# Performance work log

Measured on AMD Instinct MI355X. Metric: run time of the kernel, lower is better.

## Reference

```python
import jax, jax.numpy as jnp
import numpy as np
import math

D_MODEL, D_K, D_V, H = 512, 64, 64, 8

def setup_inputs() -> dict:
    key = jax.random.key(0)
    ks = jax.random.split(key, 8)
    B, L = 2, 4096
    q = jax.random.normal(ks[0], (B, L, D_MODEL), dtype=jnp.float32)
    k = jax.random.normal(ks[1], (B, L, D_MODEL), dtype=jnp.float32)
    v = jax.random.normal(ks[2], (B, L, D_MODEL), dtype=jnp.float32)
    attention_mask = jnp.ones((B, L), dtype=jnp.int32)
    s = 1.0 / math.sqrt(D_MODEL)
    Wq = jax.random.uniform(ks[3], (D_MODEL, H * D_K), dtype=jnp.float32, minval=-s, maxval=s)
    Wk = jax.random.uniform(ks[4], (D_MODEL, H * D_K), dtype=jnp.float32, minval=-s, maxval=s)
    Wv = jax.random.uniform(ks[5], (D_MODEL, H * D_V), dtype=jnp.float32, minval=-s, maxval=s)
    so = 1.0 / math.sqrt(H * D_V)
    Wo = jax.random.uniform(ks[6], (H * D_V, D_MODEL), dtype=jnp.float32, minval=-so, maxval=so)
    return {"q": q, "k": k, "v": v, "attention_mask": attention_mask,
            "Wq": Wq, "Wk": Wk, "Wv": Wv, "Wo": Wo}

def reference(q, k, v, attention_mask, Wq, Wk, Wv, Wo):
    B, L, _ = q.shape
    scale = 1.0 / math.sqrt(D_K)
    # project and split heads: [B, H, L, d]
    qh = (q @ Wq).reshape(B, L, H, D_K).transpose(0, 2, 1, 3)
    kh = (k @ Wk).reshape(B, L, H, D_K).transpose(0, 2, 1, 3)
    vh = (v @ Wv).reshape(B, L, H, D_V).transpose(0, 2, 1, 3)
    score = jnp.einsum('bhqd,bhkd->bhqk', qh, kh) * scale  # [B,H,L,L]
    mask = attention_mask[:, None, None, :]  # [B,1,1,L]
    score = jnp.where(mask == 0, -jnp.inf, score)
    attn = jax.nn.softmax(score, axis=-1)
    out = jnp.einsum('bhqk,bhkd->bhqd', attn, vh)
    out = out.transpose(0, 2, 1, 3).reshape(B, L, H * D_V)
    return out @ Wo
```

## Files before the change

kernel.cpp:

```cpp
#include <hip/hip_runtime.h>

typedef short bf16x8 __attribute__((ext_vector_type(8)));
typedef float f32x4 __attribute__((ext_vector_type(4)));
typedef unsigned short u16x8 __attribute__((ext_vector_type(8)));

static __device__ __forceinline__ unsigned short f2bf(float f) {
  unsigned int x = __builtin_bit_cast(unsigned int, f);
  x += 0x7FFFu + ((x >> 16) & 1u);
  return (unsigned short)(x >> 16);
}
static __device__ __forceinline__ unsigned int pk2bf(float a, float b) {
  unsigned int ia = __builtin_bit_cast(unsigned int, a) + 0x8000u;
  unsigned int ib = __builtin_bit_cast(unsigned int, b) + 0x8000u;
  return __builtin_amdgcn_perm(ib, ia, 0x07060302u);
}
static __device__ __forceinline__ void gl2lds16(const unsigned short* g, unsigned short* l) {
  __builtin_amdgcn_global_load_lds(
      (const __attribute__((address_space(1))) unsigned int*)g,
      (__attribute__((address_space(3))) unsigned int*)l, 16, 0, 0);
}

__global__ __launch_bounds__(256) void cvt3(const float* __restrict__ q, const float* __restrict__ k,
                                            const float* __restrict__ v,
                                            unsigned short* __restrict__ qo, unsigned short* __restrict__ ko,
                                            unsigned short* __restrict__ vo) {
  const float* src = (blockIdx.y == 0) ? q : (blockIdx.y == 1) ? k : v;
  unsigned short* dst = (blockIdx.y == 0) ? qo : (blockIdx.y == 1) ? ko : vo;
  int i = (blockIdx.x * 256 + threadIdx.x) * 8;
  float4 a = *(const float4*)(src + i);
  float4 b = *(const float4*)(src + i + 4);
  uint4 pk;
  pk.x = pk2bf(a.x, a.y); pk.y = pk2bf(a.z, a.w);
  pk.z = pk2bf(b.x, b.y); pk.w = pk2bf(b.z, b.w);
  *(uint4*)(dst + i) = pk;
}

__global__ __launch_bounds__(256) void wtrans4(const float* __restrict__ Wq, const float* __restrict__ Wk,
                                               const float* __restrict__ Wv, const float* __restrict__ Wo,
                                               unsigned short* __restrict__ WT) {
  __shared__ __align__(16) float T[64 * 68];
  const int z = blockIdx.z;
  const float* W = (z == 0) ? Wq : (z == 1) ? Wk : (z == 2) ? Wv : Wo;
  unsigned short* out = WT + (size_t)z * 512 * 512;
  const int k0 = blockIdx.x * 64, n0 = blockIdx.y * 64;
  const int tid = threadIdx.x;
#pragma unroll
  for (int i = 0; i < 4; ++i) {
    int chunk = i * 256 + tid;
    int row = chunk >> 4, fc = chunk & 15;
    *(float4*)(T + row * 68 + fc * 4) =
        *(const float4*)(W + (size_t)(k0 + row) * 512 + n0 + fc * 4);
  }
  __syncthreads();
#pragma unroll
  for (int i = 0; i < 2; ++i) {
    int chunk = i * 256 + tid;
    int nr = chunk >> 3, kc = chunk & 7;
    u16x8 v;
#pragma unroll
    for (int j = 0; j < 8; ++j) v[j] = f2bf(T[(kc * 8 + j) * 68 + nr]);
    *(u16x8*)(out + (size_t)(n0 + nr) * 512 + k0 + kc * 8) = v;
  }
}

__global__ __launch_bounds__(256) void gemm_qkv(const unsigned short* __restrict__ Aq,
                                                const unsigned short* __restrict__ Ak,
                                                const unsigned short* __restrict__ Av,
                                                const unsigned short* __restrict__ Bt,
                                                unsigned short* __restrict__ C,
                                                float qscale) {
  __shared__ __align__(16) unsigned short Abuf[2][128 * 64];
  __shared__ __align__(16) unsigned short Bbuf[2][64 * 64];
  const int K = 512, LDC = 1536;
  const unsigned short* A = (blockIdx.y < 8) ? Aq : (blockIdx.y < 16) ? Ak : Av;
  const float scale = (blockIdx.y < 8) ? qscale : 1.0f;
  const int tid = threadIdx.x;
  const int wid = tid >> 6, lane = tid & 63, quad = lane >> 4, li = lane & 15;
  const int bm = blockIdx.x * 128, bn = blockIdx.y * 64;
  const int wm = wid * 32;
  const unsigned short* ga[4]; int oa[4];
  const unsigned short* gb[2]; int ob[2];
#pragma unroll
  for (int i = 0; i < 4; ++i) {
    int lam = i * 256 + wid * 64 + lane;
    int r = lam >> 3, c = (lam & 7) ^ (r & 7);
    ga[i] = A + (size_t)(bm + r) * K + c * 8;
    oa[i] = lam * 8;
  }
#pragma unroll
  for (int i = 0; i < 2; ++i) {
    int lam = i * 256 + wid * 64 + lane;
    int r = lam >> 3, c = (lam & 7) ^ (r & 7);
    gb[i] = Bt + (size_t)(bn + r) * K + c * 8;
    ob[i] = lam * 8;
  }
#pragma unroll
  for (int i = 0; i < 4; ++i) { gl2lds16(ga[i], &Abuf[0][oa[i]]); ga[i] += 64; }
#pragma unroll
  for (int i = 0; i < 2; ++i) { gl2lds16(gb[i], &Bbuf[0][ob[i]]); gb[i] += 64; }

  f32x4 acc[2][4] = {};
  const int sw = li & 7;
  for (int s = 0; s < 8; ++s) {
    __builtin_amdgcn_s_barrier();
    if (s + 1 < 8) {
      int p = (s + 1) & 1;
#pragma unroll
      for (int i = 0; i < 4; ++i) { gl2lds16(ga[i], &Abuf[p][oa[i]]); ga[i] += 64; }
#pragma unroll
      for (int i = 0; i < 2; ++i) { gl2lds16(gb[i], &Bbuf[p][ob[i]]); gb[i] += 64; }
      asm volatile("s_waitcnt vmcnt(6)" ::: "memory");
    } else {
      asm volatile("s_waitcnt vmcnt(0)" ::: "memory");
    }
    __builtin_amdgcn_s_barrier();
    __builtin_amdgcn_sched_barrier(0);
    const unsigned short* As = &Abuf[s & 1][0];
    const unsigned short* Bs = &Bbuf[s & 1][0];
#pragma unroll
    for (int kk = 0; kk < 2; ++kk) {
      bf16x8 af[2], bfr[4];
#pragma unroll
      for (int t = 0; t < 2; ++t)
        af[t] = *(const bf16x8*)(As + (wm + t * 16 + li) * 64 + (((kk * 4 + quad) ^ sw) * 8));
#pragma unroll
      for (int t = 0; t < 4; ++t)
        bfr[t] = *(const bf16x8*)(Bs + (t * 16 + li) * 64 + (((kk * 4 + quad) ^ sw) * 8));
#pragma unroll
      for (int mt = 0; mt < 2; ++mt)
#pragma unroll
        for (int nt = 0; nt < 4; ++nt)
          acc[mt][nt] = __builtin_amdgcn_mfma_f32_16x16x32_bf16(af[mt], bfr[nt], acc[mt][nt], 0, 0, 0);
    }
  }
#pragma unroll
  for (int mt = 0; mt < 2; ++mt)
#pragma unroll
    for (int nt = 0; nt < 4; ++nt) {
      int r0 = bm + wm + mt * 16 + quad * 4;
      int c  = bn + nt * 16 + li;
#pragma unroll
      for (int r = 0; r < 4; ++r)
        C[(size_t)(r0 + r) * LDC + c] = f2bf(acc[mt][nt][r] * scale);
    }
}

__global__ __launch_bounds__(256) void gemm_o(const unsigned short* __restrict__ A,
                                              const unsigned short* __restrict__ Bt,
                                              float* __restrict__ Cf) {
  __shared__ __align__(16) unsigned short Abuf[2][128 * 64];
  __shared__ __align__(16) unsigned short Bbuf[2][64 * 64];
  const int K = 512, LDC = 512;
  const int tid = threadIdx.x;
  const int wid = tid >> 6, lane = tid & 63, quad = lane >> 4, li = lane & 15;
  const int bm = blockIdx.x * 128, bn = blockIdx.y * 64;
  const int wm = wid * 32;
  const unsigned short* ga[4]; int oa[4];
  const unsigned short* gb[2]; int ob[2];
#pragma unroll
  for (int i = 0; i < 4; ++i) {
    int lam = i * 256 + wid * 64 + lane;
    int r = lam >> 3, c = (lam & 7) ^ (r & 7);
    ga[i] = A + (size_t)(bm + r) * K + c * 8;
    oa[i] = lam * 8;
  }
#pragma unroll
  for (int i = 0; i < 2; ++i) {
    int lam = i * 256 + wid * 64 + lane;
    int r = lam >> 3, c = (lam & 7) ^ (r & 7);
    gb[i] = Bt + (size_t)(bn + r) * K + c * 8;
    ob[i] = lam * 8;
  }
#pragma unroll
  for (int i = 0; i < 4; ++i) { gl2lds16(ga[i], &Abuf[0][oa[i]]); ga[i] += 64; }
#pragma unroll
  for (int i = 0; i < 2; ++i) { gl2lds16(gb[i], &Bbuf[0][ob[i]]); gb[i] += 64; }

  f32x4 acc[2][4] = {};
  const int sw = li & 7;
  for (int s = 0; s < 8; ++s) {
    __builtin_amdgcn_s_barrier();
    if (s + 1 < 8) {
      int p = (s + 1) & 1;
#pragma unroll
      for (int i = 0; i < 4; ++i) { gl2lds16(ga[i], &Abuf[p][oa[i]]); ga[i] += 64; }
#pragma unroll
      for (int i = 0; i < 2; ++i) { gl2lds16(gb[i], &Bbuf[p][ob[i]]); gb[i] += 64; }
      asm volatile("s_waitcnt vmcnt(6)" ::: "memory");
    } else {
      asm volatile("s_waitcnt vmcnt(0)" ::: "memory");
    }
    __builtin_amdgcn_s_barrier();
    __builtin_amdgcn_sched_barrier(0);
    const unsigned short* As = &Abuf[s & 1][0];
    const unsigned short* Bs = &Bbuf[s & 1][0];
#pragma unroll
    for (int kk = 0; kk < 2; ++kk) {
      bf16x8 af[2], bfr[4];
#pragma unroll
      for (int t = 0; t < 2; ++t)
        af[t] = *(const bf16x8*)(As + (wm + t * 16 + li) * 64 + (((kk * 4 + quad) ^ sw) * 8));
#pragma unroll
      for (int t = 0; t < 4; ++t)
        bfr[t] = *(const bf16x8*)(Bs + (t * 16 + li) * 64 + (((kk * 4 + quad) ^ sw) * 8));
#pragma unroll
      for (int mt = 0; mt < 2; ++mt)
#pragma unroll
        for (int nt = 0; nt < 4; ++nt)
          acc[mt][nt] = __builtin_amdgcn_mfma_f32_16x16x32_bf16(af[mt], bfr[nt], acc[mt][nt], 0, 0, 0);
    }
  }
#pragma unroll
  for (int mt = 0; mt < 2; ++mt)
#pragma unroll
    for (int nt = 0; nt < 4; ++nt) {
      int r0 = bm + wm + mt * 16 + quad * 4;
      int c  = bn + nt * 16 + li;
#pragma unroll
      for (int r = 0; r < 4; ++r)
        Cf[(size_t)(r0 + r) * LDC + c] = acc[mt][nt][r];
    }
}

__global__ __launch_bounds__(256) void vtrans(const unsigned short* __restrict__ qkv,
                                              unsigned short* __restrict__ vt) {
  __shared__ __align__(16) unsigned short T[64 * 72];
  const int kt = blockIdx.x;
  const int bh = blockIdx.y;
  const int b = bh >> 3, h = bh & 7;
  const int tid = threadIdx.x;
#pragma unroll
  for (int i = 0; i < 2; ++i) {
    int chunk = i * 256 + tid;
    int row = chunk >> 3, c8 = chunk & 7;
    *(uint4*)(T + row * 72 + c8 * 8) =
        *(const uint4*)(qkv + (size_t)(b * 4096 + kt * 64 + row) * 1536 + 1024 + h * 64 + c8 * 8);
  }
  __syncthreads();
#pragma unroll
  for (int i = 0; i < 2; ++i) {
    int chunk = i * 256 + tid;
    int dr = chunk >> 3, c8 = chunk & 7;
    u16x8 v;
#pragma unroll
    for (int j = 0; j < 8; ++j) {
      int p = c8 * 8 + j;
      int ph = p & 31;
      int lk = (p & 32) | (((ph >> 2) & 1) << 4) | (((ph >> 3) & 3) << 2) | (ph & 3);
      v[j] = T[lk * 72 + dr];
    }
    *(u16x8*)(vt + (size_t)(bh * 64 + dr) * 4096 + kt * 64 + c8 * 8) = v;
  }
}

__global__ __launch_bounds__(256) void attn(const unsigned short* __restrict__ qkv,
                                            const unsigned short* __restrict__ vt,
                                            const int* __restrict__ mask,
                                            unsigned short* __restrict__ obuf) {
  __shared__ __align__(16) unsigned short Kbuf[2][64 * 64];
  __shared__ __align__(16) unsigned short Vbuf[2][64 * 64];
  __shared__ __align__(16) unsigned short MskBits[256];
  const int qt = blockIdx.x, h = blockIdx.y, b = blockIdx.z;
  const int tid = threadIdx.x;
  const int wid = tid >> 6, lane = tid & 63, quad = lane >> 4, li = lane & 15;
  const size_t tok0 = (size_t)b * 4096;

  {
    const int4* mp = (const int4*)(mask + b * 4096 + tid * 16);
    unsigned int bits = 0;
#pragma unroll
    for (int j = 0; j < 4; ++j) {
      int4 m4 = mp[j];
      bits |= (m4.x ? 1u : 0u) << (j * 4 + 0);
      bits |= (m4.y ? 1u : 0u) << (j * 4 + 1);
      bits |= (m4.z ? 1u : 0u) << (j * 4 + 2);
      bits |= (m4.w ? 1u : 0u) << (j * 4 + 3);
    }
    MskBits[tid] = (unsigned short)bits;
  }

  const unsigned short* qp0 = qkv + (tok0 + qt * 128 + wid * 32 + li) * 1536 + h * 64;
  const unsigned short* qp1 = qp0 + (size_t)16 * 1536;
  bf16x8 bq[2][2];
  bq[0][0] = *(const bf16x8*)(qp0 + quad * 8);
  bq[0][1] = *(const bf16x8*)(qp0 + 32 + quad * 8);
  bq[1][0] = *(const bf16x8*)(qp1 + quad * 8);
  bq[1][1] = *(const bf16x8*)(qp1 + 32 + quad * 8);

  const unsigned short* kbase = qkv + tok0 * 1536 + 512 + h * 64;
  const unsigned short* vbase = vt + (size_t)(b * 8 + h) * 64 * 4096;
  const int l0 = tid,       sr0 = l0 >> 3, sc0 = (l0 & 7) ^ (sr0 & 7);
  const int l1 = 256 + tid, sr1 = l1 >> 3, sc1 = (l1 & 7) ^ (sr1 & 7);
  const unsigned short* gk0 = kbase + (size_t)sr0 * 1536 + sc0 * 8;
  const unsigned short* gk1 = kbase + (size_t)sr1 * 1536 + sc1 * 8;
  const unsigned short* gv0 = vbase + (size_t)sr0 * 4096 + sc0 * 8;
  const unsigned short* gv1 = vbase + (size_t)sr1 * 4096 + sc1 * 8;
  const int ok0 = l0 * 8, ok1 = l1 * 8;

  gl2lds16(gk0, &Kbuf[0][ok0]); gl2lds16(gk1, &Kbuf[0][ok1]);
  gl2lds16(gv0, &Vbuf[0][ok0]); gl2lds16(gv1, &Vbuf[0][ok1]);
  gk0 += (size_t)64 * 1536; gk1 += (size_t)64 * 1536; gv0 += 64; gv1 += 64;

  f32x4 lacc[2] = {};
  f32x4 accO[2][4] = {};
  const int sw = li & 7;

  asm volatile("s_waitcnt lgkmcnt(0)" ::: "memory");

  for (int t = 0; t < 64; ++t) {
    __builtin_amdgcn_s_barrier();
    if (t < 63) {
      int p = (t + 1) & 1;
      gl2lds16(gk0, &Kbuf[p][ok0]); gl2lds16(gk1, &Kbuf[p][ok1]);
      gl2lds16(gv0, &Vbuf[p][ok0]); gl2lds16(gv1, &Vbuf[p][ok1]);
      gk0 += (size_t)64 * 1536; gk1 += (size_t)64 * 1536; gv0 += 64; gv1 += 64;
      asm volatile("s_waitcnt vmcnt(4)" ::: "memory");
    } else {
      asm volatile("s_waitcnt vmcnt(0)" ::: "memory");
    }
    __builtin_amdgcn_s_barrier();
    __builtin_amdgcn_sched_barrier(0);
    const unsigned short* Ks = &Kbuf[t & 1][0];
    const unsigned short* Vs = &Vbuf[t & 1][0];

    f32x4 s[2][4];
    __builtin_amdgcn_s_setprio(1);
#pragma unroll
    for (int kb = 0; kb < 4; ++kb) {
      const unsigned short* kr = Ks + (kb * 16 + li) * 64;
      bf16x8 ak0 = *(const bf16x8*)(kr + ((quad ^ sw) * 8));
      bf16x8 ak1 = *(const bf16x8*)(kr + (((4 + quad) ^ sw) * 8));
#pragma unroll
      for (int qg = 0; qg < 2; ++qg) {
        f32x4 z = {};
        z = __builtin_amdgcn_mfma_f32_16x16x32_bf16(ak0, bq[qg][0], z, 0, 0, 0);
        z = __builtin_amdgcn_mfma_f32_16x16x32_bf16(ak1, bq[qg][1], z, 0, 0, 0);
        s[qg][kb] = z;
      }
    }
    __builtin_amdgcn_s_setprio(0);
    unsigned long long mbits = *(const unsigned long long*)(MskBits + t * 4);
    if (mbits != ~0ull) {
#pragma unroll
      for (int kb = 0; kb < 4; ++kb)
#pragma unroll
        for (int r = 0; r < 4; ++r) {
          int key = kb * 16 + quad * 4 + r;
          if (!((mbits >> key) & 1ull)) { s[0][kb][r] = -1e30f; s[1][kb][r] = -1e30f; }
        }
    }
    bf16x8 pf[2][2];
#pragma unroll
    for (int qg = 0; qg < 2; ++qg) {
#pragma unroll
      for (int kb = 0; kb < 4; ++kb) {
#pragma unroll
        for (int r = 0; r < 4; ++r) s[qg][kb][r] = __builtin_amdgcn_exp2f(s[qg][kb][r]);
        lacc[qg] += s[qg][kb];
      }
      uint4 u0, u1;
      u0.x = pk2bf(s[qg][0][0], s[qg][0][1]); u0.y = pk2bf(s[qg][0][2], s[qg][0][3]);
      u0.z = pk2bf(s[qg][1][0], s[qg][1][1]); u0.w = pk2bf(s[qg][1][2], s[qg][1][3]);
      u1.x = pk2bf(s[qg][2][0], s[qg][2][1]); u1.y = pk2bf(s[qg][2][2], s[qg][2][3]);
      u1.z = pk2bf(s[qg][3][0], s[qg][3][1]); u1.w = pk2bf(s[qg][3][2], s[qg][3][3]);
      pf[qg][0] = __builtin_bit_cast(bf16x8, u0);
      pf[qg][1] = __builtin_bit_cast(bf16x8, u1);
    }
    __builtin_amdgcn_s_setprio(1);
#pragma unroll
    for (int dc = 0; dc < 4; ++dc) {
      const unsigned short* vr = Vs + (dc * 16 + li) * 64;
      bf16x8 bv0 = *(const bf16x8*)(vr + ((quad ^ sw) * 8));
      bf16x8 bv1 = *(const bf16x8*)(vr + (((4 + quad) ^ sw) * 8));
#pragma unroll
      for (int qg = 0; qg < 2; ++qg) {
        accO[qg][dc] = __builtin_amdgcn_mfma_f32_16x16x32_bf16(pf[qg][0], bv0, accO[qg][dc], 0, 0, 0);
        accO[qg][dc] = __builtin_amdgcn_mfma_f32_16x16x32_bf16(pf[qg][1], bv1, accO[qg][dc], 0, 0, 0);
      }
    }
    __builtin_amdgcn_s_setprio(0);
  }
#pragma unroll
  for (int qg = 0; qg < 2; ++qg) {
    float lt = lacc[qg][0] + lacc[qg][1] + lacc[qg][2] + lacc[qg][3];
    lt += __shfl_xor(lt, 16);
    lt += __shfl_xor(lt, 32);
    float lv0 = 1.f / __shfl(lt, quad * 4 + 0);
    float lv1 = 1.f / __shfl(lt, quad * 4 + 1);
    float lv2 = 1.f / __shfl(lt, quad * 4 + 2);
    float lv3 = 1.f / __shfl(lt, quad * 4 + 3);
    size_t r0q = tok0 + qt * 128 + wid * 32 + qg * 16 + quad * 4;
#pragma unroll
    for (int dc = 0; dc < 4; ++dc) {
      size_t col = h * 64 + dc * 16 + li;
      obuf[(r0q + 0) * 512 + col] = f2bf(accO[qg][dc][0] * lv0);
      obuf[(r0q + 1) * 512 + col] = f2bf(accO[qg][dc][1] * lv1);
      obuf[(r0q + 2) * 512 + col] = f2bf(accO[qg][dc][2] * lv2);
      obuf[(r0q + 3) * 512 + col] = f2bf(accO[qg][dc][3] * lv3);
    }
  }
}

extern "C" void kernel_launch(void* const* d_in, const int* in_sizes, int n_in,
                              void* d_out, int out_size, void* d_ws, size_t ws_size,
                              hipStream_t stream) {
  const float* q  = (const float*)d_in[0];
  const float* k  = (const float*)d_in[1];
  const float* v  = (const float*)d_in[2];
  const int* mask = (const int*)d_in[3];
  const float* Wq = (const float*)d_in[4];
  const float* Wk = (const float*)d_in[5];
  const float* Wv = (const float*)d_in[6];
  const float* Wo = (const float*)d_in[7];
  float* out = (float*)d_out;

  char* ws = (char*)d_ws;
  const size_t SA = (size_t)8192 * 512 * 2;
  unsigned short* qbf  = (unsigned short*)(ws);
  unsigned short* kbf  = (unsigned short*)(ws + SA);
  unsigned short* vbf  = (unsigned short*)(ws + 2 * SA);
  unsigned short* qkvh = (unsigned short*)(ws + 3 * SA);
  unsigned short* wAll = (unsigned short*)(ws + 6 * SA);
  unsigned short* woT  = wAll + (size_t)3 * 512 * 512;
  unsigned short* vtb  = qbf;
  unsigned short* ob   = kbf;

  dim3 cg(2048, 3);
  cvt3<<<cg, 256, 0, stream>>>(q, k, v, qbf, kbf, vbf);
  dim3 wg(8, 8, 4);
  wtrans4<<<wg, 256, 0, stream>>>(Wq, Wk, Wv, Wo, wAll);
  const float qscale = 0.125f * 1.44269504f;
  dim3 gq(64, 24);
  gemm_qkv<<<gq, 256, 0, stream>>>(qbf, kbf, vbf, wAll, qkvh, qscale);
  dim3 vg(64, 16);
  vtrans<<<vg, 256, 0, stream>>>(qkvh, vtb);
  dim3 ag(32, 8, 2);
  attn<<<ag, 256, 0, stream>>>(qkvh, vtb, mask, ob);
  dim3 go(64, 8);
  gemm_o<<<go, 256, 0, stream>>>(ob, woT, out);
}
```

Baseline: 243.2 us.

## Split attention key range across two wave halves with LDS reduction

The attention block grows from 256 to 512 threads. The second group of four waves handles the second half of the key sequence for the same 128 queries, which halves the serial loop length per wave. Partial output accumulators and row sums are combined through shared memory at the end. The grid is small (512 blocks), so this doubles the waves per CU to use more of the device. The cost is a larger LDS footprint, an extra reduction step with barriers, and more register pressure under launch_bounds(512,4).

```diff
diff --git a/kernel.cpp b/kernel.cpp
--- a/kernel.cpp
+++ b/kernel.cpp
@@ -253,19 +253,22 @@
   }
 }
 
-__global__ __launch_bounds__(256) void attn(const unsigned short* __restrict__ qkv,
-                                            const unsigned short* __restrict__ vt,
-                                            const int* __restrict__ mask,
-                                            unsigned short* __restrict__ obuf) {
-  __shared__ __align__(16) unsigned short Kbuf[2][64 * 64];
-  __shared__ __align__(16) unsigned short Vbuf[2][64 * 64];
-  __shared__ __align__(16) unsigned short MskBits[256];
+__global__ __launch_bounds__(512, 4) void attn(const unsigned short* __restrict__ qkv,
+                                               const unsigned short* __restrict__ vt,
+                                               const int* __restrict__ mask,
+                                               unsigned short* __restrict__ obuf) {
+  __shared__ __align__(16) unsigned short SM[33024];
+  unsigned short* Kb = SM;
+  unsigned short* Vb = SM + 16384;
+  unsigned short* Mk = SM + 32768;
   const int qt = blockIdx.x, h = blockIdx.y, b = blockIdx.z;
   const int tid = threadIdx.x;
   const int wid = tid >> 6, lane = tid & 63, quad = lane >> 4, li = lane & 15;
+  const int hv = wid >> 2;
+  const int wq = wid & 3;
   const size_t tok0 = (size_t)b * 4096;
 
-  {
+  if (tid < 256) {
     const int4* mp = (const int4*)(mask + b * 4096 + tid * 16);
     unsigned int bits = 0;
 #pragma unroll
@@ -276,10 +279,10 @@
       bits |= (m4.z ? 1u : 0u) << (j * 4 + 2);
       bits |= (m4.w ? 1u : 0u) << (j * 4 + 3);
     }
-    MskBits[tid] = (unsigned short)bits;
-  }
-
-  const unsigned short* qp0 = qkv + (tok0 + qt * 128 + wid * 32 + li) * 1536 + h * 64;
+    Mk[tid] = (unsigned short)bits;
+  }
+
+  const unsigned short* qp0 = qkv + (tok0 + qt * 128 + wq * 32 + li) * 1536 + h * 64;
   const unsigned short* qp1 = qp0 + (size_t)16 * 1536;
   bf16x8 bq[2][2];
   bq[0][0] = *(const bf16x8*)(qp0 + quad * 8);
@@ -289,16 +292,15 @@
 
   const unsigned short* kbase = qkv + tok0 * 1536 + 512 + h * 64;
   const unsigned short* vbase = vt + (size_t)(b * 8 + h) * 64 * 4096;
-  const int l0 = tid,       sr0 = l0 >> 3, sc0 = (l0 & 7) ^ (sr0 & 7);
-  const int l1 = 256 + tid, sr1 = l1 >> 3, sc1 = (l1 & 7) ^ (sr1 & 7);
-  const unsigned short* gk0 = kbase + (size_t)sr0 * 1536 + sc0 * 8;
-  const unsigned short* gk1 = kbase + (size_t)sr1 * 1536 + sc1 * 8;
-  const unsigned short* gv0 = vbase + (size_t)sr0 * 4096 + sc0 * 8;
-  const unsigned short* gv1 = vbase + (size_t)sr1 * 4096 + sc1 * 8;
-  const int ok0 = l0 * 8, ok1 = l1 * 8;
-
-  gl2lds16(gk0, &Kbuf[0][ok0]); gl2lds16(gk1, &Kbuf[0][ok1]);
-  gl2lds16(gv0, &Vbuf[0][ok0]); gl2lds16(gv1, &Vbuf[0][ok1]);
+  const int sr = tid >> 3, sc8 = ((tid & 7) ^ (sr & 7)) * 8;
+  const unsigned short* gk0 = kbase + (size_t)sr * 1536 + sc8;
+  const unsigned short* gk1 = kbase + (size_t)(2048 + sr) * 1536 + sc8;
+  const unsigned short* gv0 = vbase + (size_t)sr * 4096 + sc8;
+  const unsigned short* gv1 = vbase + (size_t)sr * 4096 + 2048 + sc8;
+  const int ol = tid * 8;
+
+  gl2lds16(gk0, Kb + ol);          gl2lds16(gk1, Kb + 4096 + ol);
+  gl2lds16(gv0, Vb + ol);          gl2lds16(gv1, Vb + 4096 + ol);
   gk0 += (size_t)64 * 1536; gk1 += (size_t)64 * 1536; gv0 += 64; gv1 += 64;
 
   f32x4 lacc[2] = {};
@@ -307,12 +309,14 @@
 
   asm volatile("s_waitcnt lgkmcnt(0)" ::: "memory");
 
-  for (int t = 0; t < 64; ++t) {
-    __builtin_amdgcn_s_barrier();
-    if (t < 63) {
+  for (int t = 0; t < 32; ++t) {
+    __builtin_amdgcn_s_barrier();
+    if (t < 31) {
       int p = (t + 1) & 1;
-      gl2lds16(gk0, &Kbuf[p][ok0]); gl2lds16(gk1, &Kbuf[p][ok1]);
-      gl2lds16(gv0, &Vbuf[p][ok0]); gl2lds16(gv1, &Vbuf[p][ok1]);
+      unsigned short* kd = Kb + p * 8192;
+      unsigned short* vd = Vb + p * 8192;
+      gl2lds16(gk0, kd + ol);        gl2lds16(gk1, kd + 4096 + ol);
+      gl2lds16(gv0, vd + ol);        gl2lds16(gv1, vd + 4096 + ol);
       gk0 += (size_t)64 * 1536; gk1 += (size_t)64 * 1536; gv0 += 64; gv1 += 64;
       asm volatile("s_waitcnt vmcnt(4)" ::: "memory");
     } else {
@@ -320,8 +324,8 @@
     }
     __builtin_amdgcn_s_barrier();
     __builtin_amdgcn_sched_barrier(0);
-    const unsigned short* Ks = &Kbuf[t & 1][0];
-    const unsigned short* Vs = &Vbuf[t & 1][0];
+    const unsigned short* Ks = Kb + (t & 1) * 8192 + hv * 4096;
+    const unsigned short* Vs = Vb + (t & 1) * 8192 + hv * 4096;
 
     f32x4 s[2][4];
     __builtin_amdgcn_s_setprio(1);
@@ -339,7 +343,8 @@
       }
     }
     __builtin_amdgcn_s_setprio(0);
-    unsigned long long mbits = *(const unsigned long long*)(MskBits + t * 4);
+    int tt = hv * 32 + t;
+    unsigned long long mbits = *(const unsigned long long*)(Mk + tt * 4);
     if (mbits != ~0ull) {
 #pragma unroll
       for (int kb = 0; kb < 4; ++kb)
@@ -380,23 +385,53 @@
     }
     __builtin_amdgcn_s_setprio(0);
   }
-#pragma unroll
-  for (int qg = 0; qg < 2; ++qg) {
-    float lt = lacc[qg][0] + lacc[qg][1] + lacc[qg][2] + lacc[qg][3];
-    lt += __shfl_xor(lt, 16);
-    lt += __shfl_xor(lt, 32);
-    float lv0 = 1.f / __shfl(lt, quad * 4 + 0);
-    float lv1 = 1.f / __shfl(lt, quad * 4 + 1);
-    float lv2 = 1.f / __shfl(lt, quad * 4 + 2);
-    float lv3 = 1.f / __shfl(lt, quad * 4 + 3);
-    size_t r0q = tok0 + qt * 128 + wid * 32 + qg * 16 + quad * 4;
-#pragma unroll
-    for (int dc = 0; dc < 4; ++dc) {
-      size_t col = h * 64 + dc * 16 + li;
-      obuf[(r0q + 0) * 512 + col] = f2bf(accO[qg][dc][0] * lv0);
-      obuf[(r0q + 1) * 512 + col] = f2bf(accO[qg][dc][1] * lv1);
-      obuf[(r0q + 2) * 512 + col] = f2bf(accO[qg][dc][2] * lv2);
-      obuf[(r0q + 3) * 512 + col] = f2bf(accO[qg][dc][3] * lv3);
+
+  __syncthreads();
+  float* scr = (float*)SM;
+  if (hv == 1) {
+#pragma unroll
+    for (int qg = 0; qg < 2; ++qg) {
+#pragma unroll
+      for (int dc = 0; dc < 4; ++dc)
+#pragma unroll
+        for (int r = 0; r < 4; ++r)
+          scr[(qg * 16 + dc * 4 + r) * 256 + wq * 64 + lane] = accO[qg][dc][r];
+#pragma unroll
+      for (int r = 0; r < 4; ++r)
+        scr[(32 + qg * 4 + r) * 256 + wq * 64 + lane] = lacc[qg][r];
+    }
+  }
+  __syncthreads();
+  if (hv == 0) {
+#pragma unroll
+    for (int qg = 0; qg < 2; ++qg) {
+#pragma unroll
+      for (int dc = 0; dc < 4; ++dc)
+#pragma unroll
+        for (int r = 0; r < 4; ++r)
+          accO[qg][dc][r] += scr[(qg * 16 + dc * 4 + r) * 256 + wq * 64 + lane];
+#pragma unroll
+      for (int r = 0; r < 4; ++r)
+        lacc[qg][r] += scr[(32 + qg * 4 + r) * 256 + wq * 64 + lane];
+    }
+#pragma unroll
+    for (int qg = 0; qg < 2; ++qg) {
+      float lt = lacc[qg][0] + lacc[qg][1] + lacc[qg][2] + lacc[qg][3];
+      lt += __shfl_xor(lt, 16);
+      lt += __shfl_xor(lt, 32);
+      float lv0 = 1.f / __shfl(lt, quad * 4 + 0);
+      float lv1 = 1.f / __shfl(lt, quad * 4 + 1);
+      float lv2 = 1.f / __shfl(lt, quad * 4 + 2);
+      float lv3 = 1.f / __shfl(lt, quad * 4 + 3);
+      size_t r0q = tok0 + qt * 128 + wq * 32 + qg * 16 + quad * 4;
+#pragma unroll
+      for (int dc = 0; dc < 4; ++dc) {
+        size_t col = h * 64 + dc * 16 + li;
+        obuf[(r0q + 0) * 512 + col] = f2bf(accO[qg][dc][0] * lv0);
+        obuf[(r0q + 1) * 512 + col] = f2bf(accO[qg][dc][1] * lv1);
+        obuf[(r0q + 2) * 512 + col] = f2bf(accO[qg][dc][2] * lv2);
+        obuf[(r0q + 3) * 512 + col] = f2bf(accO[qg][dc][3] * lv3);
+      }
     }
   }
 }
@@ -435,7 +470,7 @@
   dim3 vg(64, 16);
   vtrans<<<vg, 256, 0, stream>>>(qkvh, vtb);
   dim3 ag(32, 8, 2);
-  attn<<<ag, 256, 0, stream>>>(qkvh, vtb, mask, ob);
+  attn<<<ag, 512, 0, stream>>>(qkvh, vtb, mask, ob);
   dim3 go(64, 8);
   gemm_o<<<go, 256, 0, stream>>>(ob, woT, out);
 }
```

Result: faster. 226.8 us (-6.7%).
